# Performance work log

Hardware: AMD Instinct MI355X
Metric: run time of the kernel (lower is better)

Reference implementation:

```python
import jax, jax.numpy as jnp
import numpy as np

S, B, E, H = 2048, 2, 1024, 16
D = E // H  # head dim = 64


def setup_inputs() -> dict:
    key = jax.random.key(0)
    k1, k2, k3 = jax.random.split(key, 3)
    x = jax.random.normal(k1, (S, B, E), dtype=jnp.float32)
    Wqkv = jax.random.normal(k2, (3 * E, E), dtype=jnp.float32) * (E ** -0.5)
    bqkv = jax.random.normal(k3, (3 * E,), dtype=jnp.float32) * 0.02
    return {"x": x, "Wqkv": Wqkv, "bqkv": bqkv}


def reference(x, Wqkv, bqkv):
    s, b, e = x.shape
    h, d = H, E // H
    # fused QKV projection: [S,B,E] @ [E,3E] -> [S,B,3E]
    qkv = jnp.einsum('sbe,fe->sbf', x, Wqkv) + bqkv
    q, k, v = jnp.split(qkv, 3, axis=-1)
    q = q.reshape(s, b, h, d)
    k = k.reshape(s, b, h, d)
    v = v.reshape(s, b, h, d)
    scale = 1.0 / jnp.sqrt(jnp.asarray(d, dtype=x.dtype))
    # scores: [B,H,S,S]
    scores = jnp.einsum('sbhd,tbhd->bhst', q, k) * scale
    attn = jax.nn.softmax(scores, axis=-1)
    # context: [S,B,H,D] -> [S,B,E]
    ctx = jnp.einsum('bhst,tbhd->sbhd', attn, v)
    return ctx.reshape(s, b, e)
```

## Files before the change

kernel.cpp:

```cpp
#include <hip/hip_runtime.h>

constexpr int SEQ   = 2048;
constexpr int BATCH = 2;
constexpr int EMB   = 1024;
constexpr int NH    = 16;
constexpr int HDIM  = 64;
constexpr int MROWS = SEQ * BATCH;
constexpr int KDIM  = EMB;
constexpr int NCOLS = 3 * EMB;

typedef __bf16 bf16x8 __attribute__((ext_vector_type(8)));
typedef __bf16 bf16x4 __attribute__((ext_vector_type(4)));
typedef float  f32x4  __attribute__((ext_vector_type(4)));
typedef float  f32x16 __attribute__((ext_vector_type(16)));
typedef unsigned int u32;
typedef unsigned int u32x4 __attribute__((ext_vector_type(4)));

__device__ __forceinline__ u32 cvt_pk_bf16(float lo, float hi) {
  u32 r;
  asm("v_cvt_pk_bf16_f32 %0, %1, %2" : "=v"(r) : "v"(lo), "v"(hi));
  return r;
}
__device__ __forceinline__ void pl32_swap(u32& a, u32& b) {
  asm("v_permlane32_swap_b32 %0, %1" : "+v"(a), "+v"(b));
}
__device__ __forceinline__ void g2l16(const __bf16* g, __bf16* l) {
  __builtin_amdgcn_global_load_lds(
      (const __attribute__((address_space(1))) void*)g,
      (__attribute__((address_space(3))) void*)l, 16, 0, 0);
}

constexpr int N4X = (MROWS * KDIM) / 4;
constexpr int N4W = (NCOLS * KDIM) / 4;
__global__ __launch_bounds__(256) void cvt_all(
    const float* __restrict__ x, const float* __restrict__ Wq,
    __bf16* __restrict__ Xb, __bf16* __restrict__ Wb) {
  int stride = gridDim.x * blockDim.x;
  for (int i = blockIdx.x * blockDim.x + threadIdx.x; i < N4X + N4W; i += stride) {
    const float4 v = (i < N4X) ? reinterpret_cast<const float4*>(x)[i]
                               : reinterpret_cast<const float4*>(Wq)[i - N4X];
    bf16x4 o;
    o[0] = (__bf16)v.x; o[1] = (__bf16)v.y; o[2] = (__bf16)v.z; o[3] = (__bf16)v.w;
    if (i < N4X) reinterpret_cast<bf16x4*>(Xb)[i] = o;
    else         reinterpret_cast<bf16x4*>(Wb)[i - N4X] = o;
  }
}

__global__ __launch_bounds__(256, 4) void qkv_gemm(
    const __bf16* __restrict__ Xb, const __bf16* __restrict__ Wb,
    const float* __restrict__ bqkv,
    __bf16* __restrict__ Qb, __bf16* __restrict__ Kb, __bf16* __restrict__ Vt) {
  __shared__ __attribute__((aligned(16))) __bf16 Al[2][128 * 32];
  __shared__ __attribute__((aligned(16))) __bf16 Bl[2][128 * 32];

  const int tid  = threadIdx.x;
  const int lane = tid & 63;
  const int w    = tid >> 6;
  const int wm   = w >> 1, wn = w & 1;

  const int bid  = blockIdx.x;
  const int wgid = (bid & 7) * 96 + (bid >> 3);
  const int nx   = wgid % 24;
  const int nyy  = wgid / 24;
  const int m0   = nyy * 128;
  const int n0   = nx * 128;

  f32x4 acc[4][4] = {};

  auto stage = [&](int buf, int kt) {
#pragma unroll
    for (int c = 0; c < 2; ++c) {
      const int u   = (w * 2 + c) * 64 + lane;
      const int row = u >> 2;
      const int sc  = ((u & 3) ^ ((row >> 1) & 3)) * 8;
      g2l16(&Xb[(size_t)(m0 + row) * KDIM + kt * 32 + sc], &Al[buf][(w * 2 + c) * 512]);
      g2l16(&Wb[(size_t)(n0 + row) * KDIM + kt * 32 + sc], &Bl[buf][(w * 2 + c) * 512]);
    }
  };

  stage(0, 0);
  __syncthreads();

  const int l15 = lane & 15, hi4 = lane >> 4;
  const int cswz = (hi4 ^ ((l15 >> 1) & 3)) * 8;

  for (int kt = 0; kt < KDIM / 32; ++kt) {
    const int buf = kt & 1;
    if (kt + 1 < KDIM / 32) stage(buf ^ 1, kt + 1);

    bf16x8 af[4], bfr[4];
#pragma unroll
    for (int i = 0; i < 4; ++i) {
      af[i]  = *reinterpret_cast<const bf16x8*>(&Al[buf][(wm * 64 + i * 16 + l15) * 32 + cswz]);
      bfr[i] = *reinterpret_cast<const bf16x8*>(&Bl[buf][(wn * 64 + i * 16 + l15) * 32 + cswz]);
    }
    __builtin_amdgcn_s_setprio(1);
#pragma unroll
    for (int i = 0; i < 4; ++i)
#pragma unroll
      for (int j = 0; j < 4; ++j)
        acc[i][j] = __builtin_amdgcn_mfma_f32_16x16x32_bf16(af[i], bfr[j], acc[i][j], 0, 0, 0);
    __builtin_amdgcn_s_setprio(0);
    __syncthreads();
  }

  const float QSCALE = 0.18033688011112042f;
#pragma unroll
  for (int j = 0; j < 4; ++j) {
    const int f    = n0 + wn * 64 + j * 16 + l15;
    const float bias = bqkv[f];
    const int sec  = f >> 10;
    const int hd   = f & 1023;
    const int h    = hd >> 6, d = hd & 63;
#pragma unroll
    for (int i = 0; i < 4; ++i) {
#pragma unroll
      for (int r = 0; r < 4; ++r) {
        const int mm = m0 + wm * 64 + i * 16 + hi4 * 4 + r;
        const int s_ = mm >> 1, b_ = mm & 1;
        const int bh = b_ * NH + h;
        const float val = acc[i][j][r] + bias;
        if (sec == 0) {
          Qb[((size_t)bh * SEQ + s_) * HDIM + d] = (__bf16)(val * QSCALE);
        } else if (sec == 1) {
          Kb[((size_t)bh * SEQ + s_) * HDIM + d] = (__bf16)val;
        } else {
          Vt[((size_t)bh * HDIM + d) * SEQ + s_] = (__bf16)val;
        }
      }
    }
  }
}

template <int SPLIT>
__global__ __launch_bounds__(128, 4) void attn_fwd(
    const __bf16* __restrict__ Qb, const __bf16* __restrict__ Kb,
    const __bf16* __restrict__ Vt, float* __restrict__ out,
    float* __restrict__ Op, float2* __restrict__ ml) {
  __shared__ __attribute__((aligned(16))) __bf16 lds[16384];

  const int tid  = threadIdx.x;
  const int lane = tid & 63;
  const int w    = tid >> 6;
  const int lq   = lane & 31;
  const int hi   = lane >> 5;

  const int bid = blockIdx.x;
  int bh, qi, half, t_begin, nt;
  if constexpr (SPLIT) {
    const int wgid = (bid & 7) * 256 + (bid >> 3);
    bh = wgid >> 6; qi = (wgid >> 1) & 31; half = wgid & 1;
    t_begin = half * (SEQ / 2); nt = SEQ / 128;
  } else {
    const int wgid = (bid & 7) * 128 + (bid >> 3);
    bh = wgid >> 5; qi = wgid & 31; half = 0;
    t_begin = 0; nt = SEQ / 64;
  }
  const int b_ = bh >> 4, h = bh & 15;
  const int q0 = qi * 64 + w * 32;

  const __bf16* Qp = Qb + (size_t)bh * SEQ * HDIM;
  const __bf16* Kp = Kb + (size_t)bh * SEQ * HDIM;
  const __bf16* Vp = Vt + (size_t)bh * HDIM * SEQ;

  bf16x8 qf[4];
#pragma unroll
  for (int ks = 0; ks < 4; ++ks)
    qf[ks] = *reinterpret_cast<const bf16x8*>(&Qp[(size_t)(q0 + lq) * HDIM + ks * 16 + hi * 8]);

  f32x16 acc0 = {}, acc1 = {};
  float m = -1e30f, l = 0.f;

  auto stage = [&](int b, int t0) {
#pragma unroll
    for (int c = 0; c < 4; ++c) {
      const int u   = (w * 4 + c) * 64 + lane;
      const int row = u >> 3;
      const int sc  = ((u & 7) * 8) ^ ((row & 7) << 3);
      g2l16(Kp + (size_t)(t0 + row) * HDIM + sc, lds + b * 8192 + (w * 4 + c) * 512);
      g2l16(Vp + (size_t)row * SEQ + t0 + sc,    lds + b * 8192 + 4096 + (w * 4 + c) * 512);
    }
  };

  stage(0, t_begin);
  __syncthreads();

  for (int it = 0; it < nt; ++it) {
    const int cur = it & 1;
    if (it + 1 < nt) stage(cur ^ 1, t_begin + (it + 1) * 64);
    const __bf16* kb = lds + cur * 8192;
    const __bf16* vb = kb + 4096;

    f32x16 S0 = {}, S1 = {};
    __builtin_amdgcn_s_setprio(1);
#pragma unroll
    for (int ks = 0; ks < 4; ++ks) {
      const int colb = ks * 16 + hi * 8;
      bf16x8 k0 = *reinterpret_cast<const bf16x8*>(&kb[lq * 64        + (colb ^ ((lq & 7) << 3))]);
      bf16x8 k1 = *reinterpret_cast<const bf16x8*>(&kb[(32 + lq) * 64 + (colb ^ ((lq & 7) << 3))]);
      S0 = __builtin_amdgcn_mfma_f32_32x32x16_bf16(k0, qf[ks], S0, 0, 0, 0);
      S1 = __builtin_amdgcn_mfma_f32_32x32x16_bf16(k1, qf[ks], S1, 0, 0, 0);
    }
    __builtin_amdgcn_s_setprio(0);

    float pmax;
    {
      float t0m = fmaxf(S0[0], S0[1]), t1m = fmaxf(S0[2], S0[3]);
      float t2m = fmaxf(S0[4], S0[5]), t3m = fmaxf(S0[6], S0[7]);
      float t4m = fmaxf(S0[8], S0[9]), t5m = fmaxf(S0[10], S0[11]);
      float t6m = fmaxf(S0[12], S0[13]), t7m = fmaxf(S0[14], S0[15]);
      t0m = fmaxf(t0m, t1m); t2m = fmaxf(t2m, t3m); t4m = fmaxf(t4m, t5m); t6m = fmaxf(t6m, t7m);
      float a_ = fmaxf(fmaxf(t0m, t2m), fmaxf(t4m, t6m));
      float u0 = fmaxf(S1[0], S1[1]), u1 = fmaxf(S1[2], S1[3]);
      float u2 = fmaxf(S1[4], S1[5]), u3 = fmaxf(S1[6], S1[7]);
      float u4 = fmaxf(S1[8], S1[9]), u5 = fmaxf(S1[10], S1[11]);
      float u6 = fmaxf(S1[12], S1[13]), u7 = fmaxf(S1[14], S1[15]);
      u0 = fmaxf(u0, u1); u2 = fmaxf(u2, u3); u4 = fmaxf(u4, u5); u6 = fmaxf(u6, u7);
      float b2 = fmaxf(fmaxf(u0, u2), fmaxf(u4, u6));
      pmax = fmaxf(a_, b2);
    }
    pmax = fmaxf(pmax, __shfl_xor(pmax, 32));

    if (__any(pmax > m + 8.f)) {
      const float mnew  = fmaxf(m, pmax);
      const float alpha = __builtin_amdgcn_exp2f(m - mnew);
      m = mnew;
      l *= alpha;
#pragma unroll
      for (int i = 0; i < 16; ++i) { acc0[i] *= alpha; acc1[i] *= alpha; }
    }

    float r0 = 0.f, r1 = 0.f, r2 = 0.f, r3 = 0.f;
#pragma unroll
    for (int i = 0; i < 4; ++i) {
      S0[i]      = __builtin_amdgcn_exp2f(S0[i] - m);      r0 += S0[i];
      S0[i + 4]  = __builtin_amdgcn_exp2f(S0[i + 4] - m);  r1 += S0[i + 4];
      S0[i + 8]  = __builtin_amdgcn_exp2f(S0[i + 8] - m);  r2 += S0[i + 8];
      S0[i + 12] = __builtin_amdgcn_exp2f(S0[i + 12] - m); r3 += S0[i + 12];
    }
#pragma unroll
    for (int i = 0; i < 4; ++i) {
      S1[i]      = __builtin_amdgcn_exp2f(S1[i] - m);      r0 += S1[i];
      S1[i + 4]  = __builtin_amdgcn_exp2f(S1[i + 4] - m);  r1 += S1[i + 4];
      S1[i + 8]  = __builtin_amdgcn_exp2f(S1[i + 8] - m);  r2 += S1[i + 8];
      S1[i + 12] = __builtin_amdgcn_exp2f(S1[i + 12] - m); r3 += S1[i + 12];
    }
    l += (r0 + r1) + (r2 + r3);

    bf16x8 pw[4];
    {
      auto mk = [&](const f32x16& P, bf16x8* dst) {
#pragma unroll
        for (int kk = 0; kk < 2; ++kk) {
          u32 a0 = cvt_pk_bf16(P[kk * 8 + 0], P[kk * 8 + 1]);
          u32 b0 = cvt_pk_bf16(P[kk * 8 + 4], P[kk * 8 + 5]);
          u32 a1 = cvt_pk_bf16(P[kk * 8 + 2], P[kk * 8 + 3]);
          u32 b1 = cvt_pk_bf16(P[kk * 8 + 6], P[kk * 8 + 7]);
          pl32_swap(a0, b0);
          pl32_swap(a1, b1);
          u32x4 wv; wv[0] = a0; wv[1] = a1; wv[2] = b0; wv[3] = b1;
          dst[kk] = __builtin_bit_cast(bf16x8, wv);
        }
      };
      mk(S0, &pw[0]);
      mk(S1, &pw[2]);
    }

    __builtin_amdgcn_s_setprio(1);
#pragma unroll
    for (int ks = 0; ks < 4; ++ks) {
      const int colb = ks * 16 + hi * 8;
      bf16x8 v0 = *reinterpret_cast<const bf16x8*>(&vb[lq * 64        + (colb ^ ((lq & 7) << 3))]);
      bf16x8 v1 = *reinterpret_cast<const bf16x8*>(&vb[(32 + lq) * 64 + (colb ^ ((lq & 7) << 3))]);
      acc0 = __builtin_amdgcn_mfma_f32_32x32x16_bf16(v0, pw[ks], acc0, 0, 0, 0);
      acc1 = __builtin_amdgcn_mfma_f32_32x32x16_bf16(v1, pw[ks], acc1, 0, 0, 0);
    }
    __builtin_amdgcn_s_setprio(0);

    __syncthreads();
  }

  l += __shfl_xor(l, 32);
  if constexpr (SPLIT) {
    const int rowg = (bh * 32 + qi) * 64 + w * 32 + lq;
    float* pp = Op + ((size_t)rowg * 2 + half) * 64;
#pragma unroll
    for (int rr = 0; rr < 4; ++rr) {
      float4 o0 = {acc0[4 * rr], acc0[4 * rr + 1], acc0[4 * rr + 2], acc0[4 * rr + 3]};
      *reinterpret_cast<float4*>(&pp[8 * rr + 4 * hi]) = o0;
      float4 o1 = {acc1[4 * rr], acc1[4 * rr + 1], acc1[4 * rr + 2], acc1[4 * rr + 3]};
      *reinterpret_cast<float4*>(&pp[8 * rr + 4 * hi + 32]) = o1;
    }
    if (hi == 0) ml[rowg * 2 + half] = make_float2(m, l);
  } else {
    const float inv = 1.0f / l;
    const int s_ = q0 + lq;
    float* op = out + ((size_t)s_ * BATCH + b_) * EMB + h * HDIM;
#pragma unroll
    for (int rr = 0; rr < 4; ++rr) {
      float4 o0 = {acc0[4 * rr] * inv, acc0[4 * rr + 1] * inv,
                   acc0[4 * rr + 2] * inv, acc0[4 * rr + 3] * inv};
      *reinterpret_cast<float4*>(&op[8 * rr + 4 * hi]) = o0;
      float4 o1 = {acc1[4 * rr] * inv, acc1[4 * rr + 1] * inv,
                   acc1[4 * rr + 2] * inv, acc1[4 * rr + 3] * inv};
      *reinterpret_cast<float4*>(&op[8 * rr + 4 * hi + 32]) = o1;
    }
  }
}

__global__ __launch_bounds__(256) void attn_combine(
    const float* __restrict__ Op, const float2* __restrict__ ml,
    float* __restrict__ out) {
  const int idx  = blockIdx.x * 256 + threadIdx.x;
  const int rowg = idx >> 4;
  const int c    = idx & 15;
  const float2 a = ml[rowg * 2];
  const float2 b = ml[rowg * 2 + 1];
  const float M  = fmaxf(a.x, b.x);
  const float w0 = __builtin_amdgcn_exp2f(a.x - M);
  const float w1 = __builtin_amdgcn_exp2f(b.x - M);
  const float inv = 1.0f / (a.y * w0 + b.y * w1);
  const float4 o0 = *reinterpret_cast<const float4*>(&Op[((size_t)rowg * 2) * 64 + c * 4]);
  const float4 o1 = *reinterpret_cast<const float4*>(&Op[((size_t)rowg * 2 + 1) * 64 + c * 4]);
  float4 o = {(o0.x * w0 + o1.x * w1) * inv, (o0.y * w0 + o1.y * w1) * inv,
              (o0.z * w0 + o1.z * w1) * inv, (o0.w * w0 + o1.w * w1) * inv};
  const int bh = rowg >> 11, s_ = rowg & 2047;
  const int b_ = bh >> 4, h = bh & 15;
  *reinterpret_cast<float4*>(&out[((size_t)s_ * BATCH + b_) * EMB + h * HDIM + c * 4]) = o;
}

extern "C" void kernel_launch(void* const* d_in, const int* in_sizes, int n_in,
                              void* d_out, int out_size, void* d_ws, size_t ws_size,
                              hipStream_t stream) {
  (void)in_sizes; (void)n_in; (void)out_size;
  const float* x    = (const float*)d_in[0];
  const float* Wqkv = (const float*)d_in[1];
  const float* bias = (const float*)d_in[2];
  float* out = (float*)d_out;

  char* ws = (char*)d_ws;
  __bf16* Xb = (__bf16*)(ws);
  __bf16* Wb = (__bf16*)(ws + 8388608);
  __bf16* Qb = (__bf16*)(ws + 14680064);
  __bf16* Kb = (__bf16*)(ws + 23068672);
  __bf16* Vt = (__bf16*)(ws + 31457280);
  float*  Op = (float*)(ws + 39845888);
  float2* ml = (float2*)(ws + 73400320);
  const size_t NEED = 74448896;

  cvt_all<<<dim3(2048), dim3(256), 0, stream>>>(x, Wqkv, Xb, Wb);
  qkv_gemm<<<dim3(768), dim3(256), 0, stream>>>(Xb, Wb, bias, Qb, Kb, Vt);
  if (ws_size >= NEED) {
    attn_fwd<1><<<dim3(2048), dim3(128), 0, stream>>>(Qb, Kb, Vt, out, Op, ml);
    attn_combine<<<dim3(4096), dim3(256), 0, stream>>>(Op, ml, out);
  } else {
    attn_fwd<0><<<dim3(1024), dim3(128), 0, stream>>>(Qb, Kb, Vt, out, Op, ml);
  }
}
```

Measured before the change: 123.3 us.

## Load K/V fragments directly from global memory instead of LDS double-buffering

The attention kernel no longer stages K and V tiles into shared memory with async copies and double buffering. Each wave now loads its MFMA operand fragments straight from global memory (relying on L2/L1), which removes LDS traffic and the per-iteration __syncthreads. Blocks grow to 256 threads (4 waves, 128 queries) with half as many blocks, so each block's waves share the same K/V stream through cache. The risk is higher global/L1 load latency and more redundant reads across waves, with no explicit prefetch to hide them.

New measurement: 179.2 us. +45.3%, slower.

```diff
diff --git a/kernel.cpp b/kernel.cpp
--- a/kernel.cpp
+++ b/kernel.cpp
@@ -133,12 +133,10 @@
 }
 
 template <int SPLIT>
-__global__ __launch_bounds__(128, 4) void attn_fwd(
+__global__ __launch_bounds__(256, 3) void attn_fwd(
     const __bf16* __restrict__ Qb, const __bf16* __restrict__ Kb,
     const __bf16* __restrict__ Vt, float* __restrict__ out,
     float* __restrict__ Op, float2* __restrict__ ml) {
-  __shared__ __attribute__((aligned(16))) __bf16 lds[16384];
-
   const int tid  = threadIdx.x;
   const int lane = tid & 63;
   const int w    = tid >> 6;
@@ -148,16 +146,16 @@
   const int bid = blockIdx.x;
   int bh, qi, half, t_begin, nt;
   if constexpr (SPLIT) {
-    const int wgid = (bid & 7) * 256 + (bid >> 3);
-    bh = wgid >> 6; qi = (wgid >> 1) & 31; half = wgid & 1;
+    const int wgid = (bid & 7) * 128 + (bid >> 3);
+    bh = wgid >> 5; qi = (wgid >> 1) & 15; half = wgid & 1;
     t_begin = half * (SEQ / 2); nt = SEQ / 128;
   } else {
-    const int wgid = (bid & 7) * 128 + (bid >> 3);
-    bh = wgid >> 5; qi = wgid & 31; half = 0;
+    const int wgid = (bid & 7) * 64 + (bid >> 3);
+    bh = wgid >> 4; qi = wgid & 15; half = 0;
     t_begin = 0; nt = SEQ / 64;
   }
   const int b_ = bh >> 4, h = bh & 15;
-  const int q0 = qi * 64 + w * 32;
+  const int q0 = qi * 128 + w * 32;
 
   const __bf16* Qp = Qb + (size_t)bh * SEQ * HDIM;
   const __bf16* Kp = Kb + (size_t)bh * SEQ * HDIM;
@@ -168,40 +166,37 @@
   for (int ks = 0; ks < 4; ++ks)
     qf[ks] = *reinterpret_cast<const bf16x8*>(&Qp[(size_t)(q0 + lq) * HDIM + ks * 16 + hi * 8]);
 
+  const __bf16* kf0 = Kp + ((size_t)(t_begin + lq) * HDIM + hi * 8);
+  const __bf16* kf1 = kf0 + 32 * HDIM;
+  const __bf16* vf0 = Vp + ((size_t)lq * SEQ + t_begin + hi * 8);
+  const __bf16* vf1 = vf0 + 32 * SEQ;
+
   f32x16 acc0 = {}, acc1 = {};
   float m = -1e30f, l = 0.f;
 
-  auto stage = [&](int b, int t0) {
-#pragma unroll
-    for (int c = 0; c < 4; ++c) {
-      const int u   = (w * 4 + c) * 64 + lane;
-      const int row = u >> 3;
-      const int sc  = ((u & 7) * 8) ^ ((row & 7) << 3);
-      g2l16(Kp + (size_t)(t0 + row) * HDIM + sc, lds + b * 8192 + (w * 4 + c) * 512);
-      g2l16(Vp + (size_t)row * SEQ + t0 + sc,    lds + b * 8192 + 4096 + (w * 4 + c) * 512);
-    }
-  };
-
-  stage(0, t_begin);
-  __syncthreads();
-
   for (int it = 0; it < nt; ++it) {
-    const int cur = it & 1;
-    if (it + 1 < nt) stage(cur ^ 1, t_begin + (it + 1) * 64);
-    const __bf16* kb = lds + cur * 8192;
-    const __bf16* vb = kb + 4096;
-
     f32x16 S0 = {}, S1 = {};
+    bf16x8 k0[4], k1[4], v0[4], v1[4];
+#pragma unroll
+    for (int ks = 0; ks < 4; ++ks) {
+      k0[ks] = *reinterpret_cast<const bf16x8*>(kf0 + ks * 16);
+      k1[ks] = *reinterpret_cast<const bf16x8*>(kf1 + ks * 16);
+    }
     __builtin_amdgcn_s_setprio(1);
 #pragma unroll
     for (int ks = 0; ks < 4; ++ks) {
-      const int colb = ks * 16 + hi * 8;
-      bf16x8 k0 = *reinterpret_cast<const bf16x8*>(&kb[lq * 64        + (colb ^ ((lq & 7) << 3))]);
-      bf16x8 k1 = *reinterpret_cast<const bf16x8*>(&kb[(32 + lq) * 64 + (colb ^ ((lq & 7) << 3))]);
-      S0 = __builtin_amdgcn_mfma_f32_32x32x16_bf16(k0, qf[ks], S0, 0, 0, 0);
-      S1 = __builtin_amdgcn_mfma_f32_32x32x16_bf16(k1, qf[ks], S1, 0, 0, 0);
+      S0 = __builtin_amdgcn_mfma_f32_32x32x16_bf16(k0[ks], qf[ks], S0, 0, 0, 0);
+      S1 = __builtin_amdgcn_mfma_f32_32x32x16_bf16(k1[ks], qf[ks], S1, 0, 0, 0);
     }
     __builtin_amdgcn_s_setprio(0);
+
+#pragma unroll
+    for (int ks = 0; ks < 4; ++ks) {
+      v0[ks] = *reinterpret_cast<const bf16x8*>(vf0 + ks * 16);
+      v1[ks] = *reinterpret_cast<const bf16x8*>(vf1 + ks * 16);
+    }
+    kf0 += 64 * HDIM; kf1 += 64 * HDIM;
+    vf0 += 64; vf1 += 64;
 
     float pmax;
     {
@@ -269,20 +264,15 @@
     __builtin_amdgcn_s_setprio(1);
 #pragma unroll
     for (int ks = 0; ks < 4; ++ks) {
-      const int colb = ks * 16 + hi * 8;
-      bf16x8 v0 = *reinterpret_cast<const bf16x8*>(&vb[lq * 64        + (colb ^ ((lq & 7) << 3))]);
-      bf16x8 v1 = *reinterpret_cast<const bf16x8*>(&vb[(32 + lq) * 64 + (colb ^ ((lq & 7) << 3))]);
-      acc0 = __builtin_amdgcn_mfma_f32_32x32x16_bf16(v0, pw[ks], acc0, 0, 0, 0);
-      acc1 = __builtin_amdgcn_mfma_f32_32x32x16_bf16(v1, pw[ks], acc1, 0, 0, 0);
+      acc0 = __builtin_amdgcn_mfma_f32_32x32x16_bf16(v0[ks], pw[ks], acc0, 0, 0, 0);
+      acc1 = __builtin_amdgcn_mfma_f32_32x32x16_bf16(v1[ks], pw[ks], acc1, 0, 0, 0);
     }
     __builtin_amdgcn_s_setprio(0);
-
-    __syncthreads();
   }
 
   l += __shfl_xor(l, 32);
   if constexpr (SPLIT) {
-    const int rowg = (bh * 32 + qi) * 64 + w * 32 + lq;
+    const int rowg = bh * SEQ + q0 + lq;
     float* pp = Op + ((size_t)rowg * 2 + half) * 64;
 #pragma unroll
     for (int rr = 0; rr < 4; ++rr) {
@@ -351,9 +341,9 @@
   cvt_all<<<dim3(2048), dim3(256), 0, stream>>>(x, Wqkv, Xb, Wb);
   qkv_gemm<<<dim3(768), dim3(256), 0, stream>>>(Xb, Wb, bias, Qb, Kb, Vt);
   if (ws_size >= NEED) {
-    attn_fwd<1><<<dim3(2048), dim3(128), 0, stream>>>(Qb, Kb, Vt, out, Op, ml);
+    attn_fwd<1><<<dim3(1024), dim3(256), 0, stream>>>(Qb, Kb, Vt, out, Op, ml);
     attn_combine<<<dim3(4096), dim3(256), 0, stream>>>(Op, ml, out);
   } else {
-    attn_fwd<0><<<dim3(1024), dim3(128), 0, stream>>>(Qb, Kb, Vt, out, Op, ml);
-  }
-}
+    attn_fwd<0><<<dim3(512), dim3(256), 0, stream>>>(Qb, Kb, Vt, out, Op, ml);
+  }
+}
```
